# Kernel optimization log

Hardware: AMD Instinct MI355X
Metric: run time of the kernel (lower is better)

The kernel has to match this reference:

```python
import jax, jax.numpy as jnp
import numpy as np
from jax import lax

WINDOW = 11
SIGMA = 1.5
CHANNELS = 3
DATA_RANGE = 1.0
WEIGHTS = (0.0448, 0.2856, 0.3001, 0.2363, 0.1333)


def _gaussian_kernel_2d(size, sigma, channels):
    x = np.arange(size, dtype=np.float32) - size // 2
    k1 = np.exp(-x ** 2 / (2 * sigma ** 2))
    k1 = k1 / k1.sum()
    k2 = np.outer(k1, k1)
    k2 = k2 / k2.sum()
    return jnp.asarray(np.tile(k2[None, None], (channels, 1, 1, 1)), dtype=jnp.float32)


def _depthwise_blur(x, kernel):
    # x: [B, G, H, W], kernel: [C, 1, kh, kw] tiled to G groups
    groups = x.shape[1]
    reps = groups // kernel.shape[0]
    k = jnp.tile(kernel, (reps, 1, 1, 1))
    return lax.conv_general_dilated(
        x, k, window_strides=(1, 1), padding='SAME',
        feature_group_count=groups,
        dimension_numbers=('NCHW', 'OIHW', 'NCHW'))


def _avg_pool2(x):
    b, c, h, w = x.shape
    return x.reshape(b, c, h // 2, 2, w // 2, 2).mean(axis=(3, 5))


def _ssim_components(pred, target, kernel):
    C1 = (0.01 * DATA_RANGE) ** 2
    C2 = (0.03 * DATA_RANGE) ** 2
    # Fuse the 5 depthwise blurs into a single grouped conv over stacked channels
    stacked = jnp.concatenate(
        [pred, target, pred * pred, target * target, pred * target], axis=1)
    blurred = _depthwise_blur(stacked, kernel)
    mu1, mu2, e_pp, e_tt, e_pt = jnp.split(blurred, 5, axis=1)
    mu1_sq = mu1 * mu1
    mu2_sq = mu2 * mu2
    mu1_mu2 = mu1 * mu2
    sigma1_sq = jnp.maximum(e_pp - mu1_sq, 0.0)
    sigma2_sq = jnp.maximum(e_tt - mu2_sq, 0.0)
    sigma12 = e_pt - mu1_mu2
    l = (2 * mu1_mu2 + C1) / (mu1_sq + mu2_sq + C1)
    cs = (2 * sigma12 + C2) / (sigma1_sq + sigma2_sq + C2)
    return l.mean(), cs.mean()


def setup_inputs() -> dict:
    key = jax.random.key(0)
    k1, k2 = jax.random.split(key)
    pred = jax.random.uniform(k1, (16, 3, 512, 512), dtype=jnp.float32)
    target = jax.random.uniform(k2, (16, 3, 512, 512), dtype=jnp.float32)
    kernel = _gaussian_kernel_2d(WINDOW, SIGMA, CHANNELS)
    return {'pred': pred, 'target': target, 'kernel': kernel}


def reference(pred, target, kernel):
    weights = jnp.asarray(WEIGHTS, dtype=pred.dtype)
    msssim = jnp.ones((1,), dtype=pred.dtype)
    n_scales = len(WEIGHTS)
    for i in range(n_scales):
        if i > 0:
            pred = _avg_pool2(pred)
            target = _avg_pool2(target)
        if pred.shape[2] < WINDOW or pred.shape[3] < WINDOW:
            break
        l, cs = _ssim_components(pred, target, kernel)
        if i == n_scales - 1:
            msssim = msssim * jnp.maximum(l, 1e-8) ** weights[i] \
                            * jnp.maximum(cs, 1e-8) ** weights[i]
        else:
            msssim = msssim * jnp.maximum(cs, 1e-8) ** weights[i]
    return msssim
```

## Files before the change

kernel.cpp:

```cpp
#include <hip/hip_runtime.h>
#include <math.h>

#define NP 48

typedef float v2f __attribute__((ext_vector_type(2)));

__device__ __forceinline__ float uniform_f(float v) {
    int i = __builtin_amdgcn_readfirstlane(__builtin_bit_cast(int, v));
    return __builtin_bit_cast(float, i);
}

template<int CHF, int TAIL, int R>
__device__ __forceinline__ void ssim_scale(
        const float* __restrict__ P, const float* __restrict__ T,
        int H, int sh, int lb, int scale, int slotsel, int tid,
        const float* __restrict__ k2d, double* __restrict__ accum,
        float (*__restrict__ rows)[272])
{
    float w[11];
    {
        float s = 0.f;
#pragma unroll
        for (int i = 0; i < 11; ++i) s += k2d[55 + i];
        float inv = 1.0f / s;
#pragma unroll
        for (int i = 0; i < 11; ++i) w[i] = uniform_f(k2d[55 + i] * inv);
    }

    int blocksX = (NP << sh) >> 8;
    int bxi = lb % blocksX;
    int by  = lb / blocksX;
    int g0  = bxi << 8;
    int g   = g0 + tid;
    int pl  = g >> sh;
    int x   = g & (H - 1);
    int yb  = by * R;

    float wz[11];
#pragma unroll
    for (int j = 0; j < 11; ++j) {
        int c = x - 5 + j;
        wz[j] = (c >= 0 && c < H) ? w[j] : 0.f;
    }

    int HH   = H * H;
    int Cown = pl * HH + x;
    int gmax = (NP << sh) - 1;
    int gh   = (tid < 5) ? (g0 - 5 + tid) : (g0 + 256 + (tid - 5));
    gh = gh < 0 ? 0 : (gh > gmax ? gmax : gh);
    int Chalo = (gh >> sh) * HH + (gh & (H - 1));
    int hidx  = (tid < 5) ? tid : (256 + tid);
    bool is_halo = tid < 10;

    v2f wmu[11], we[11];
    float wpt[11];
    const float C1 = 1e-4f, C2 = 9e-4f;
    float lsum = 0.f, csum = 0.f;
    int rr = yb - 5;

    {
        int nr = rr < 0 ? 0 : rr;
        int ro = nr * H;
        rows[0][5 + tid] = P[Cown + ro];
        rows[2][5 + tid] = T[Cown + ro];
        if (is_halo) {
            rows[0][hidx] = P[Chalo + ro];
            rows[2][hidx] = T[Chalo + ro];
        }
        __syncthreads();
    }

#define SSIM_STEP(PH)                                                          \
    {                                                                          \
        const int cb = (PH) & 1;               \
        const int sl = (PH) % 11;              \
                      \
        int nr = rr + 1;                                                       \
        nr = nr < 0 ? 0 : nr;                                                  \
        nr = nr > H - 1 ? H - 1 : nr;                                          \
        int ro = nr * H;                                                       \
        float vp = P[Cown + ro], vt = T[Cown + ro];                            \
        float hp = 0.f, ht = 0.f;                                              \
        if (is_halo) { hp = P[Chalo + ro]; ht = T[Chalo + ro]; }               \
            \
        v2f a_mu = (v2f){0.f, 0.f};                                            \
        v2f a_e  = (v2f){0.f, 0.f};                                            \
        float apt = 0.f;                                                       \
        if (rr >= 0 && rr < H) {                            \
            _Pragma("unroll")                                                  \
            for (int j = 0; j < 11; ++j) {                                     \
                float pj = rows[cb][tid + j];                                  \
                float tj = rows[2 + cb][tid + j];                              \
                v2f pt2 = (v2f){pj, tj};                                       \
                v2f wv  = (v2f){wz[j], wz[j]};                                 \
                v2f wp2 = wv * pt2;                                            \
                a_mu += wp2;                                                   \
                a_e  += wp2 * pt2;                                             \
                apt = fmaf(wp2.x, tj, apt);                    \
            }                                                                  \
        }                                                                      \
        wmu[sl] = a_mu; we[sl] = a_e; wpt[sl] = apt;                           \
        if (rr >= yb + 5) {                          \
            v2f mu2 = (v2f){0.f, 0.f};                                         \
            v2f e2  = (v2f){0.f, 0.f};                                         \
            float ept = 0.f;                                                   \
            _Pragma("unroll")                                                  \
            for (int i = 0; i < 11; ++i) {                                     \
                const int ss = (sl + 1 + i) % 11;            \
                v2f wi = (v2f){w[i], w[i]};                \
                mu2 += wi * wmu[ss];                                           \
                e2  += wi * we[ss];                                            \
                ept = fmaf(w[i], wpt[ss], ept);                                \
            }                                                                  \
            float m11 = mu2.x * mu2.x, m22 = mu2.y * mu2.y, m12 = mu2.x * mu2.y; \
            float s1  = fmaxf(e2.x - m11, 0.f);                                \
            float s2  = fmaxf(e2.y - m22, 0.f);                                \
            float s12 = ept - m12;                                             \
            lsum += (2.f * m12 + C1) * __builtin_amdgcn_rcpf(m11 + m22 + C1);  \
            csum += (2.f * s12 + C2) * __builtin_amdgcn_rcpf(s1 + s2 + C2);    \
        }                                                                      \
          \
                               \
        rows[cb ^ 1][5 + tid] = vp;                                            \
        rows[2 + (cb ^ 1)][5 + tid] = vt;                                      \
        if (is_halo) { rows[cb ^ 1][hidx] = hp; rows[2 + (cb ^ 1)][hidx] = ht; } \
        __syncthreads();                                                       \
        rr++;                                                                  \
    }

#pragma unroll 1
    for (int ch = 0; ch < CHF; ++ch) {
#pragma unroll
        for (int ph = 0; ph < 22; ++ph) SSIM_STEP(ph)
    }
#pragma unroll
    for (int ph = 0; ph < TAIL; ++ph) SSIM_STEP(ph)
#undef SSIM_STEP

#pragma unroll
    for (int o = 32; o > 0; o >>= 1) {
        lsum += __shfl_down(lsum, o, 64);
        csum += __shfl_down(csum, o, 64);
    }
    __shared__ float red[8];
    int wv = tid >> 6;
    if ((tid & 63) == 0) { red[2 * wv] = lsum; red[2 * wv + 1] = csum; }
    __syncthreads();
    if (tid == 0) {
        int slot = (scale * 8 + slotsel) * 2;
        atomicAdd(&accum[slot],     (double)(red[0] + red[2] + red[4] + red[6]));
        atomicAdd(&accum[slot + 1], (double)(red[1] + red[3] + red[5] + red[7]));
    }
}

__device__ __forceinline__ void pool_job(int b, int tid,
        const float* __restrict__ pred, const float* __restrict__ targ,
        float* __restrict__ p1, float* __restrict__ t1,
        float* __restrict__ p2, float* __restrict__ t2,
        float* __restrict__ p3, float* __restrict__ t3,
        float* __restrict__ p4, float* __restrict__ t4)
{
    int pi   = b >> 4;
    int tile = b & 15;
    int pls  = pi < 48 ? pi : pi - 48;
    const float* src = (pi < 48 ? pred : targ) + (size_t)pls * 512 * 512;
    float* d1 = (pi < 48 ? p1 : t1) + (size_t)pls * 256 * 256;
    float* d2 = (pi < 48 ? p2 : t2) + (size_t)pls * 128 * 128;
    float* d3 = (pi < 48 ? p3 : t3) + (size_t)pls * 64 * 64;
    float* d4 = (pi < 48 ? p4 : t4) + (size_t)pls * 32 * 32;
    int tY = tile >> 2, tX = tile & 3;
    int ty = tid >> 4, tx = tid & 15;
    int gy0 = tY * 128 + ty * 8, gx0 = tX * 128 + tx * 8;

    float s1v[4][4];
#pragma unroll
    for (int i = 0; i < 4; ++i) {
        const float* r0 = src + (size_t)(gy0 + 2 * i) * 512 + gx0;
        const float* r1 = r0 + 512;
        float4 a0 = *(const float4*)r0, a1 = *(const float4*)(r0 + 4);
        float4 b0 = *(const float4*)r1, b1 = *(const float4*)(r1 + 4);
        s1v[i][0] = 0.25f * ((a0.x + a0.y) + (b0.x + b0.y));
        s1v[i][1] = 0.25f * ((a0.z + a0.w) + (b0.z + b0.w));
        s1v[i][2] = 0.25f * ((a1.x + a1.y) + (b1.x + b1.y));
        s1v[i][3] = 0.25f * ((a1.z + a1.w) + (b1.z + b1.w));
        *(float4*)(d1 + (size_t)(tY * 64 + ty * 4 + i) * 256 + tX * 64 + tx * 4) =
            *(float4*)s1v[i];
    }
    float s2v[2][2];
#pragma unroll
    for (int i = 0; i < 2; ++i) {
#pragma unroll
        for (int j = 0; j < 2; ++j)
            s2v[i][j] = 0.25f * ((s1v[2*i][2*j] + s1v[2*i][2*j+1]) +
                                 (s1v[2*i+1][2*j] + s1v[2*i+1][2*j+1]));
        *(float2*)(d2 + (size_t)(tY * 32 + ty * 2 + i) * 128 + tX * 32 + tx * 2) =
            *(float2*)s2v[i];
    }
    float s3 = 0.25f * ((s2v[0][0] + s2v[0][1]) + (s2v[1][0] + s2v[1][1]));
    d3[(size_t)(tY * 16 + ty) * 64 + tX * 16 + tx] = s3;
    float v1 = s3 + __shfl_xor(s3, 1, 64);
    float v2 = v1 + __shfl_xor(v1, 16, 64);
    if ((ty & 1) == 0 && (tx & 1) == 0)
        d4[(size_t)(tY * 8 + (ty >> 1)) * 32 + tX * 8 + (tx >> 1)] = 0.25f * v2;
}

__global__ __launch_bounds__(256) void k_A(
        const float* __restrict__ pred, const float* __restrict__ targ,
        float* __restrict__ p1, float* __restrict__ t1,
        float* __restrict__ p2, float* __restrict__ t2,
        float* __restrict__ p3, float* __restrict__ t3,
        float* __restrict__ p4, float* __restrict__ t4,
        const float* __restrict__ k2d, double* __restrict__ accum)
{
    __shared__ float rows[4][272];
    int b   = blockIdx.x;
    int tid = threadIdx.x;
    if (b < 768) {
        ssim_scale<3, 8, 64>(pred, targ, 512, 9, b, 0, b & 7, tid, k2d, accum, rows);
    } else {
        pool_job(b - 768, tid, pred, targ, p1, t1, p2, t2, p3, t3, p4, t4);
    }
}

__global__ __launch_bounds__(256) void k_B(
        const float* __restrict__ p1, const float* __restrict__ t1,
        const float* __restrict__ p2, const float* __restrict__ t2,
        const float* __restrict__ p3, const float* __restrict__ t3,
        const float* __restrict__ p4, const float* __restrict__ t4,
        const float* __restrict__ k2d, double* __restrict__ accum)
{
    __shared__ float rows[4][272];
    int b   = blockIdx.x;
    int tid = threadIdx.x;
    if (b < 192)      ssim_scale<3, 8, 64>(p1, t1, 256, 8, b,       1, b & 7, tid, k2d, accum, rows);
    else if (b < 240) ssim_scale<3, 8, 64>(p2, t2, 128, 7, b - 192, 2, b & 7, tid, k2d, accum, rows);
    else if (b < 252) ssim_scale<3, 8, 64>(p3, t3, 64,  6, b - 240, 3, b & 7, tid, k2d, accum, rows);
    else              ssim_scale<1, 20, 32>(p4, t4, 32, 5, b - 252, 4, b & 7, tid, k2d, accum, rows);
}

__global__ void k_final(const double* __restrict__ accum, float* __restrict__ out) {
    if (threadIdx.x != 0 || blockIdx.x != 0) return;
    const float wts[5] = {0.0448f, 0.2856f, 0.3001f, 0.2363f, 0.1333f};
    float ms = 1.0f;
    int Hs = 512;
    for (int s = 0; s < 5; ++s) {
        double lt = 0.0, ct = 0.0;
        for (int k = 0; k < 8; ++k) {
            lt += accum[(s * 8 + k) * 2];
            ct += accum[(s * 8 + k) * 2 + 1];
        }
        float N  = 48.0f * (float)Hs * (float)Hs;
        float l  = (float)lt / N;
        float cs = fmaxf((float)ct / N, 1e-8f);
        if (s == 4) {
            l = fmaxf(l, 1e-8f);
            ms *= powf(l, wts[s]) * powf(cs, wts[s]);
        } else {
            ms *= powf(cs, wts[s]);
        }
        Hs >>= 1;
    }
    out[0] = ms;
}

extern "C" void kernel_launch(void* const* d_in, const int* in_sizes, int n_in,
                              void* d_out, int out_size, void* d_ws, size_t ws_size,
                              hipStream_t stream) {
    const float* pred = (const float*)d_in[0];
    const float* targ = (const float*)d_in[1];
    const float* kern = (const float*)d_in[2];
    float* out = (float*)d_out;

    char* ws = (char*)d_ws;
    double* accum = (double*)ws;
    size_t off = 1024;
    float* p1 = (float*)(ws + off); off += (size_t)NP * 256 * 256 * 4;
    float* t1 = (float*)(ws + off); off += (size_t)NP * 256 * 256 * 4;
    float* p2 = (float*)(ws + off); off += (size_t)NP * 128 * 128 * 4;
    float* t2 = (float*)(ws + off); off += (size_t)NP * 128 * 128 * 4;
    float* p3 = (float*)(ws + off); off += (size_t)NP * 64 * 64 * 4;
    float* t3 = (float*)(ws + off); off += (size_t)NP * 64 * 64 * 4;
    float* p4 = (float*)(ws + off); off += (size_t)NP * 32 * 32 * 4;
    float* t4 = (float*)(ws + off); off += (size_t)NP * 32 * 32 * 4;

    hipMemsetAsync(accum, 0, 640, stream);
    k_A<<<2304, 256, 0, stream>>>(pred, targ, p1, t1, p2, t2, p3, t3, p4, t4, kern, accum);
    k_B<<<258, 256, 0, stream>>>(p1, t1, p2, t2, p3, t3, p4, t4, kern, accum);
    k_final<<<1, 1, 0, stream>>>(accum, out);
}
```

Measured before the change: 232.4 us.

## Merge all stages into one persistent kernel with atomic work queue

Replaces the three launches (k_A, k_B, k_final) with a single persistent kernel whose blocks pull jobs from an atomic counter. Pool jobs come first. Later-scale SSIM jobs spin-wait on a completion counter, and the last SSIM job to finish runs the final reduction. It also splits SSIM work into smaller jobs (ssim_scale<1,20,32>, more blocks per scale) for better load balance. This removes launch gaps and the kernel-boundary barrier between scales, at the cost of spin-waiting, atomic traffic, and less work per block.

```diff
diff --git a/kernel.cpp b/kernel.cpp
--- a/kernel.cpp
+++ b/kernel.cpp
@@ -2,6 +2,15 @@
 #include <math.h>
 
 #define NP 48
+
+#define NPOOL 1536
+#define S0_BEG 1536
+#define S1_BEG 3072
+#define S2_BEG 3456
+#define S3_BEG 3552
+#define S4_BEG 3576
+#define NTOT   3582
+#define NSSIM  2046
 
 typedef float v2f __attribute__((ext_vector_type(2)));
 
@@ -82,7 +91,7 @@
         float vp = P[Cown + ro], vt = T[Cown + ro];                            \
         float hp = 0.f, ht = 0.f;                                              \
         if (is_halo) { hp = P[Chalo + ro]; ht = T[Chalo + ro]; }               \
-            \
+                           \
         v2f a_mu = (v2f){0.f, 0.f};                                            \
         v2f a_e  = (v2f){0.f, 0.f};                                            \
         float apt = 0.f;                                                       \
@@ -119,8 +128,7 @@
             lsum += (2.f * m12 + C1) * __builtin_amdgcn_rcpf(m11 + m22 + C1);  \
             csum += (2.f * s12 + C2) * __builtin_amdgcn_rcpf(s1 + s2 + C2);    \
         }                                                                      \
-          \
-                               \
+             \
         rows[cb ^ 1][5 + tid] = vp;                                            \
         rows[2 + (cb ^ 1)][5 + tid] = vt;                                      \
         if (is_halo) { rows[cb ^ 1][hidx] = hp; rows[2 + (cb ^ 1)][hidx] = ht; } \
@@ -204,50 +212,17 @@
         d4[(size_t)(tY * 8 + (ty >> 1)) * 32 + tX * 8 + (tx >> 1)] = 0.25f * v2;
 }
 
-__global__ __launch_bounds__(256) void k_A(
-        const float* __restrict__ pred, const float* __restrict__ targ,
-        float* __restrict__ p1, float* __restrict__ t1,
-        float* __restrict__ p2, float* __restrict__ t2,
-        float* __restrict__ p3, float* __restrict__ t3,
-        float* __restrict__ p4, float* __restrict__ t4,
-        const float* __restrict__ k2d, double* __restrict__ accum)
-{
-    __shared__ float rows[4][272];
-    int b   = blockIdx.x;
-    int tid = threadIdx.x;
-    if (b < 768) {
-        ssim_scale<3, 8, 64>(pred, targ, 512, 9, b, 0, b & 7, tid, k2d, accum, rows);
-    } else {
-        pool_job(b - 768, tid, pred, targ, p1, t1, p2, t2, p3, t3, p4, t4);
-    }
-}
-
-__global__ __launch_bounds__(256) void k_B(
-        const float* __restrict__ p1, const float* __restrict__ t1,
-        const float* __restrict__ p2, const float* __restrict__ t2,
-        const float* __restrict__ p3, const float* __restrict__ t3,
-        const float* __restrict__ p4, const float* __restrict__ t4,
-        const float* __restrict__ k2d, double* __restrict__ accum)
-{
-    __shared__ float rows[4][272];
-    int b   = blockIdx.x;
-    int tid = threadIdx.x;
-    if (b < 192)      ssim_scale<3, 8, 64>(p1, t1, 256, 8, b,       1, b & 7, tid, k2d, accum, rows);
-    else if (b < 240) ssim_scale<3, 8, 64>(p2, t2, 128, 7, b - 192, 2, b & 7, tid, k2d, accum, rows);
-    else if (b < 252) ssim_scale<3, 8, 64>(p3, t3, 64,  6, b - 240, 3, b & 7, tid, k2d, accum, rows);
-    else              ssim_scale<1, 20, 32>(p4, t4, 32, 5, b - 252, 4, b & 7, tid, k2d, accum, rows);
-}
-
-__global__ void k_final(const double* __restrict__ accum, float* __restrict__ out) {
-    if (threadIdx.x != 0 || blockIdx.x != 0) return;
+__device__ void finalize(double* __restrict__ accum, float* __restrict__ out) {
     const float wts[5] = {0.0448f, 0.2856f, 0.3001f, 0.2363f, 0.1333f};
     float ms = 1.0f;
     int Hs = 512;
     for (int s = 0; s < 5; ++s) {
         double lt = 0.0, ct = 0.0;
         for (int k = 0; k < 8; ++k) {
-            lt += accum[(s * 8 + k) * 2];
-            ct += accum[(s * 8 + k) * 2 + 1];
+            lt += __hip_atomic_load(&accum[(s * 8 + k) * 2],
+                                    __ATOMIC_RELAXED, __HIP_MEMORY_SCOPE_AGENT);
+            ct += __hip_atomic_load(&accum[(s * 8 + k) * 2 + 1],
+                                    __ATOMIC_RELAXED, __HIP_MEMORY_SCOPE_AGENT);
         }
         float N  = 48.0f * (float)Hs * (float)Hs;
         float l  = (float)lt / N;
@@ -263,6 +238,71 @@
     out[0] = ms;
 }
 
+__global__ __launch_bounds__(256) void k_all(
+        const float* __restrict__ pred, const float* __restrict__ targ,
+        float* __restrict__ p1, float* __restrict__ t1,
+        float* __restrict__ p2, float* __restrict__ t2,
+        float* __restrict__ p3, float* __restrict__ t3,
+        float* __restrict__ p4, float* __restrict__ t4,
+        const float* __restrict__ k2d, double* __restrict__ accum,
+        unsigned* __restrict__ ctl, float* __restrict__ out)
+{
+    __shared__ float rows[4][272];
+    __shared__ unsigned sj;
+    int tid = threadIdx.x;
+
+    for (;;) {
+        __syncthreads();
+        if (tid == 0) sj = atomicAdd(&ctl[0], 1u);
+        __syncthreads();
+        unsigned j = sj;
+        if (j >= NTOT) break;
+
+        if (j < NPOOL) {
+            pool_job((int)j, tid, pred, targ, p1, t1, p2, t2, p3, t3, p4, t4);
+            __syncthreads();
+            if (tid == 0) {
+                __threadfence();
+                atomicAdd(&ctl[1], 1u);
+            }
+        } else {
+            if (j >= S1_BEG) {
+                if (tid == 0) {
+                    while (__hip_atomic_load(&ctl[1], __ATOMIC_ACQUIRE,
+                                             __HIP_MEMORY_SCOPE_AGENT) < NPOOL)
+                        __builtin_amdgcn_s_sleep(8);
+                    __threadfence();
+                }
+                __syncthreads();
+            }
+            if (j < S1_BEG)
+                ssim_scale<1, 20, 32>(pred, targ, 512, 9, (int)(j - S0_BEG), 0,
+                                      j & 7, tid, k2d, accum, rows);
+            else if (j < S2_BEG)
+                ssim_scale<1, 20, 32>(p1, t1, 256, 8, (int)(j - S1_BEG), 1,
+                                      j & 7, tid, k2d, accum, rows);
+            else if (j < S3_BEG)
+                ssim_scale<1, 20, 32>(p2, t2, 128, 7, (int)(j - S2_BEG), 2,
+                                      j & 7, tid, k2d, accum, rows);
+            else if (j < S4_BEG)
+                ssim_scale<1, 20, 32>(p3, t3, 64, 6, (int)(j - S3_BEG), 3,
+                                      j & 7, tid, k2d, accum, rows);
+            else
+                ssim_scale<1, 20, 32>(p4, t4, 32, 5, (int)(j - S4_BEG), 4,
+                                      j & 7, tid, k2d, accum, rows);
+
+            if (tid == 0) {
+                __threadfence();
+                unsigned d = atomicAdd(&ctl[2], 1u);
+                if (d == NSSIM - 1) {
+                    __threadfence();
+                    finalize(accum, out);
+                }
+            }
+        }
+    }
+}
+
 extern "C" void kernel_launch(void* const* d_in, const int* in_sizes, int n_in,
                               void* d_out, int out_size, void* d_ws, size_t ws_size,
                               hipStream_t stream) {
@@ -273,6 +313,7 @@
 
     char* ws = (char*)d_ws;
     double* accum = (double*)ws;
+    unsigned* ctl = (unsigned*)(ws + 768);
     size_t off = 1024;
     float* p1 = (float*)(ws + off); off += (size_t)NP * 256 * 256 * 4;
     float* t1 = (float*)(ws + off); off += (size_t)NP * 256 * 256 * 4;
@@ -283,8 +324,7 @@
     float* p4 = (float*)(ws + off); off += (size_t)NP * 32 * 32 * 4;
     float* t4 = (float*)(ws + off); off += (size_t)NP * 32 * 32 * 4;
 
-    hipMemsetAsync(accum, 0, 640, stream);
-    k_A<<<2304, 256, 0, stream>>>(pred, targ, p1, t1, p2, t2, p3, t3, p4, t4, kern, accum);
-    k_B<<<258, 256, 0, stream>>>(p1, t1, p2, t2, p3, t3, p4, t4, kern, accum);
-    k_final<<<1, 1, 0, stream>>>(accum, out);
-}
+    hipMemsetAsync(ws, 0, 1024, stream);
+    k_all<<<2048, 256, 0, stream>>>(pred, targ, p1, t1, p2, t2, p3, t3, p4, t4,
+                                    kern, accum, ctl, out);
+}
```

New measurement: 708.0 us. 205% more time.
